# Performance work log

Hardware: AMD Instinct MI355X
Metric: run time of the kernel (lower is better)

The kernel has to match this reference:

```python
import jax, jax.numpy as jnp
import numpy as np

# ---- Haar DWT (levels=1, mode='zero'), matches pytorch_wavelets ordering ----
# For even H,W and filter length 2, zero-pad haar analysis reduces to
# non-overlapping 2x2 blocks. Subband order after the two 1D analyses
# (width first, then height): LL, (w-lo,h-hi), (w-hi,h-lo), HH.

def haar_dwt(x):
    a = x[..., 0::2, 0::2]
    b = x[..., 0::2, 1::2]
    c = x[..., 1::2, 0::2]
    d = x[..., 1::2, 1::2]
    ll = (a + b + c + d) * 0.5
    h0 = (a + b - c - d) * 0.5   # lo-width, hi-height
    h1 = (a - b + c - d) * 0.5   # hi-width, lo-height
    hh = (a - b - c + d) * 0.5
    return ll, jnp.stack([h0, h1, hh], axis=2)  # yh: (b,c,3,h/2,w/2)


def _interleave(u, v, axis):
    # interleave two equal-shaped arrays along `axis` (negative axis)
    s = list(u.shape)
    s[axis] *= 2
    return jnp.stack([u, v], axis=axis + len(u.shape) + 1).reshape(s)


def haar_idwt(ll, yh):
    h0, h1, hh = yh[:, :, 0], yh[:, :, 1], yh[:, :, 2]
    a = (ll + h0 + h1 + hh) * 0.5
    b = (ll + h0 - h1 - hh) * 0.5
    c = (ll - h0 + h1 - hh) * 0.5
    d = (ll - h0 - h1 + hh) * 0.5
    top = _interleave(a, b, -1)   # even rows
    bot = _interleave(c, d, -1)   # odd rows
    return _interleave(top, bot, -2)


def batched_dynamic_conv(feat, kernels, pad):
    """feat: (b,cin,h,w), kernels: (b,cout,cin,kh,kw) -> (b,cout,h,w).
    Per-sample kernels via grouped conv (batch as groups)."""
    bsz, cin, h, w = feat.shape
    cout, kh, kw = kernels.shape[1], kernels.shape[3], kernels.shape[4]
    lhs = feat.reshape(1, bsz * cin, h, w)
    rhs = kernels.reshape(bsz * cout, cin, kh, kw)
    out = jax.lax.conv_general_dilated(
        lhs, rhs, window_strides=(1, 1), padding=[(pad, pad), (pad, pad)],
        dimension_numbers=('NCHW', 'OIHW', 'NCHW'), feature_group_count=bsz)
    return out.reshape(bsz, cout, h, w)


def _dyn_conv_subband(feat, sub_kernels, attn_w, attn_b, pad=1):
    # attention: 1x1 conv -> global avg pool -> softmax over kernel_num
    logits = jnp.einsum('bchw,kc->bk', feat, attn_w) / (feat.shape[-2] * feat.shape[-1]) + attn_b
    att = jax.nn.softmax(logits, axis=1)                       # (b,K)
    kernels = jnp.einsum('bk,koiuv->boiuv', att, sub_kernels)  # (b,cout,cin,kh,kw)
    return batched_dynamic_conv(feat, kernels, pad)


def setup_inputs() -> dict:
    key = jax.random.key(0)
    k1, k2, k3, k4 = jax.random.split(key, 4)
    B, C, H, W = 8, 64, 128, 128
    K, SUB, COUT, KS = 4, 4, 64, 3  # kernel_num, 1+3*levels, out_channels, kernel_size
    return {
        'x': jax.random.normal(k1, (B, C, H, W), dtype=jnp.float32),
        'wt_kernels': jax.random.normal(k2, (K, SUB, COUT, C, KS, KS), dtype=jnp.float32) * 0.02,
        'attn_w': jax.random.normal(k3, (K, C), dtype=jnp.float32) * 0.1,
        'attn_b': jnp.zeros((K,), dtype=jnp.float32),
    }


def reference(x, wt_kernels, attn_w, attn_b):
    ll, yh = haar_dwt(x)
    subbands = [ll, yh[:, :, 0], yh[:, :, 1], yh[:, :, 2]]
    outs = [_dyn_conv_subband(sb, wt_kernels[:, i], attn_w, attn_b, pad=1)
            for i, sb in enumerate(subbands)]
    rec_yh = jnp.stack(outs[1:4], axis=2)  # (b,cout,3,h/2,w/2)
    return haar_idwt(outs[0], rec_yh)
```

## Files before the change

kernel.cpp:

```cpp
#include <hip/hip_runtime.h>
#include <hip/hip_bf16.h>
#include <math.h>


typedef __bf16 bf16x8 __attribute__((ext_vector_type(8)));
typedef float f32x4 __attribute__((ext_vector_type(4)));

__device__ __forceinline__ bf16x8 as_bf16x8(uint4 u) {
    union { uint4 a; bf16x8 b; } c; c.a = u; return c.b;
}
__device__ __forceinline__ unsigned short bf16bits(float f) {
    __hip_bfloat16 h = __float2bfloat16(f);
    union { __hip_bfloat16 h; unsigned short u; } c; c.h = h; return c.u;
}

__global__ __launch_bounds__(256)
void dwt_kernel(const float* __restrict__ x, const float* __restrict__ attn_w,
                unsigned short* __restrict__ feats, float* __restrict__ plog) {
    __shared__ uint4 sT[2304];
    __shared__ float sred[64][4];
    unsigned short* sTu = (unsigned short*)sT;
    int y = blockIdx.x, b = blockIdx.y;
    int t = threadIdx.x;
    int c = t >> 2, q = t & 3;

    const float4* r0 = (const float4*)x + ((size_t)(b * 64 + c) * 128 + 2 * y) * 32;
    const float4* r1 = r0 + 32;

    float s0 = 0.f, s1 = 0.f, s2 = 0.f, s3 = 0.f;
    #pragma unroll
    for (int i = 0; i < 8; ++i) {
        int f = i * 4 + q;
        float4 p = r0[f], qq = r1[f];
        int xo = 2 * f;
        {
            float a = p.x, bb = p.y, cc = qq.x, dd = qq.y;
            float ll = (a + bb + cc + dd) * 0.5f, h0 = (a + bb - cc - dd) * 0.5f;
            float h1 = (a - bb + cc - dd) * 0.5f, hh = (a - bb - cc + dd) * 0.5f;
            s0 += ll; s1 += h0; s2 += h1; s3 += hh;
            sTu[0 * 4608 + xo * 72 + c] = bf16bits(ll);
            sTu[1 * 4608 + xo * 72 + c] = bf16bits(h0);
            sTu[2 * 4608 + xo * 72 + c] = bf16bits(h1);
            sTu[3 * 4608 + xo * 72 + c] = bf16bits(hh);
        }
        {
            float a = p.z, bb = p.w, cc = qq.z, dd = qq.w;
            float ll = (a + bb + cc + dd) * 0.5f, h0 = (a + bb - cc - dd) * 0.5f;
            float h1 = (a - bb + cc - dd) * 0.5f, hh = (a - bb - cc + dd) * 0.5f;
            s0 += ll; s1 += h0; s2 += h1; s3 += hh;
            sTu[0 * 4608 + (xo + 1) * 72 + c] = bf16bits(ll);
            sTu[1 * 4608 + (xo + 1) * 72 + c] = bf16bits(h0);
            sTu[2 * 4608 + (xo + 1) * 72 + c] = bf16bits(h1);
            sTu[3 * 4608 + (xo + 1) * 72 + c] = bf16bits(hh);
        }
    }
    s0 += __shfl_xor(s0, 1); s0 += __shfl_xor(s0, 2);
    s1 += __shfl_xor(s1, 1); s1 += __shfl_xor(s1, 2);
    s2 += __shfl_xor(s2, 1); s2 += __shfl_xor(s2, 2);
    s3 += __shfl_xor(s3, 1); s3 += __shfl_xor(s3, 2);
    if (q == 0) { sred[c][0] = s0; sred[c][1] = s1; sred[c][2] = s2; sred[c][3] = s3; }
    __syncthreads();
    if (t < 16) {
        int sub = t >> 2, k = t & 3;
        float acc = 0.f;
        #pragma unroll 8
        for (int cc = 0; cc < 64; ++cc)
            acc += attn_w[k * 64 + cc] * sred[cc][sub];
        plog[((size_t)(b * 4 + sub) * 4 + k) * 64 + y] = acc;
    }
    uint4* fch = (uint4*)feats;
    for (int e = t; e < 2048; e += 256) {
        int s = e >> 9, xx = (e >> 3) & 63, ck = e & 7;
        fch[(size_t)((b * 4 + s) * 64 + y) * 512 + xx * 8 + ck] = sT[s * 576 + xx * 9 + ck];
    }
}

__global__ __launch_bounds__(256)
void mix_kernel(const float* __restrict__ wt, const float* __restrict__ attn_b,
                const float* __restrict__ plog, unsigned short* __restrict__ wmix) {
    __shared__ float sLw[4][576];
    __shared__ float satt[8][4];
    int co = blockIdx.x, sub = blockIdx.y;
    int t = threadIdx.x;

    if (t < 32) {
        int b = t >> 2, k = t & 3;
        const float* pp = plog + ((size_t)(b * 4 + sub) * 4 + k) * 64;
        float acc = 0.f;
        #pragma unroll 8
        for (int yy = 0; yy < 64; ++yy) acc += pp[yy];
        float logit = acc * (1.0f / 4096.0f) + attn_b[k];
        float m = fmaxf(logit, __shfl_xor(logit, 1));
        m = fmaxf(m, __shfl_xor(m, 2));
        float e = expf(logit - m);
        float s = e + __shfl_xor(e, 1);
        s += __shfl_xor(s, 2);
        satt[b][k] = e / s;
    }
    for (int e = t; e < 2304; e += 256) {
        int k = e / 576, r = e - k * 576;
        sLw[k][r] = wt[((size_t)(k * 4 + sub) * 64 + co) * 576 + r];
    }
    __syncthreads();
    #pragma unroll
    for (int j = 0; j < 18; ++j) {
        int idx = j * 256 + t;
        int b = idx / 576;
        int r = idx - b * 576;
        int tap = r >> 6, ci = r & 63;
        int wi = ci * 9 + tap;
        float v = satt[b][0] * sLw[0][wi] + satt[b][1] * sLw[1][wi]
                + satt[b][2] * sLw[2][wi] + satt[b][3] * sLw[3][wi];
        wmix[((size_t)(b * 4 + sub) * 9 + tap) * 4096 + co * 64 + ci] = bf16bits(v);
    }
}

__global__ __launch_bounds__(256, 2)
void conv_idwt_kernel(const unsigned short* __restrict__ feats,
                      const unsigned short* __restrict__ wmix,
                      float* __restrict__ out) {
    __shared__ uint4 sA[2592];
    __shared__ uint4 sW[1152];
    int cg = blockIdx.x, tile = blockIdx.y, b = blockIdx.z;
    int y0 = (tile >> 2) * 16, x0 = (tile & 3) * 16;
    int t = threadIdx.x, w = t >> 6, l = t & 63;
    int l16 = l & 15, kg = l >> 4;
    int w4 = w * 4;
    const uint4* fchb = (const uint4*)feats + (size_t)b * 131072;
    const uint4* wchb = (const uint4*)wmix + (size_t)b * 18432;

    f32x4 acc[4][4];
    #pragma unroll
    for (int s = 0; s < 4; ++s)
        #pragma unroll
        for (int r = 0; r < 4; ++r)
            acc[s][r] = (f32x4){0.f, 0.f, 0.f, 0.f};

    #pragma unroll
    for (int sp = 0; sp < 2; ++sp) {
        #pragma unroll
        for (int ck8 = 0; ck8 < 8; ck8 += 4) {
            __syncthreads();
            for (int e = t; e < 2592; e += 256) {
                int s2 = e / 1296, rr = e - s2 * 1296;
                int py = rr / 72, r2 = rr - py * 72, px = r2 >> 2, g = r2 & 3;
                int gy = y0 - 1 + py, gx = x0 - 1 + px;
                uint4 v = make_uint4(0u, 0u, 0u, 0u);
                if ((unsigned)gy < 64u && (unsigned)gx < 64u)
                    v = fchb[(size_t)(sp * 2 + s2) * 32768 + (gy * 64 + gx) * 8 + ck8 + g];
                sA[e] = v;
            }
            for (int e = t; e < 1152; e += 256) {
                int s2 = e / 576, r = e - s2 * 576;
                int tap = r >> 6, co = (r >> 2) & 15, g = r & 3;
                sW[e] = wchb[(size_t)(sp * 2 + s2) * 4608 + tap * 512
                             + (cg * 16 + co) * 8 + ck8 + g];
            }
            __syncthreads();
            #pragma unroll
            for (int s2 = 0; s2 < 2; ++s2) {
                int s = sp * 2 + s2;
                int abase = s2 * 1296;
                uint4 af[4][3];
                #pragma unroll
                for (int i = 0; i < 4; ++i)
                    #pragma unroll
                    for (int dx = 0; dx < 3; ++dx)
                        af[i][dx] = sA[abase + ((w4 + i) * 18 + l16 + dx) * 4 + kg];
                #pragma unroll
                for (int dy = 0; dy < 3; ++dy) {
                    if (dy > 0) {
                        #pragma unroll
                        for (int i = 0; i < 3; ++i)
                            #pragma unroll
                            for (int dx = 0; dx < 3; ++dx)
                                af[i][dx] = af[i + 1][dx];
                        #pragma unroll
                        for (int dx = 0; dx < 3; ++dx)
                            af[3][dx] = sA[abase + ((w4 + dy + 3) * 18 + l16 + dx) * 4 + kg];
                    }
                    #pragma unroll
                    for (int dx = 0; dx < 3; ++dx) {
                        uint4 bw = sW[s2 * 576 + (dy * 3 + dx) * 64 + l16 * 4 + kg];
                        bf16x8 bfr = as_bf16x8(bw);
                        #pragma unroll
                        for (int r = 0; r < 4; ++r)
                            acc[s][r] = __builtin_amdgcn_mfma_f32_16x16x32_bf16(
                                as_bf16x8(af[r][dx]), bfr, acc[s][r], 0, 0, 0);
                    }
                }
            }
        }
    }
    int co = cg * 16 + l16;
    #pragma unroll
    for (int r = 0; r < 4; ++r) {
        int ys = y0 + w4 + r;
        float* orow = out + ((size_t)(b * 64 + co) * 128 + 2 * ys) * 128 + 2 * x0 + 8 * kg;
        float av[4], bv[4], cv[4], dv[4];
        #pragma unroll
        for (int j = 0; j < 4; ++j) {
            float ll = acc[0][r][j], h0 = acc[1][r][j];
            float h1 = acc[2][r][j], hh = acc[3][r][j];
            av[j] = (ll + h0 + h1 + hh) * 0.5f;
            bv[j] = (ll + h0 - h1 - hh) * 0.5f;
            cv[j] = (ll - h0 + h1 - hh) * 0.5f;
            dv[j] = (ll - h0 - h1 + hh) * 0.5f;
        }
        *(float4*)(orow)           = make_float4(av[0], bv[0], av[1], bv[1]);
        *(float4*)(orow + 4)       = make_float4(av[2], bv[2], av[3], bv[3]);
        *(float4*)(orow + 128)     = make_float4(cv[0], dv[0], cv[1], dv[1]);
        *(float4*)(orow + 132)     = make_float4(cv[2], dv[2], cv[3], dv[3]);
    }
}

extern "C" void kernel_launch(void* const* d_in, const int* in_sizes, int n_in,
                              void* d_out, int out_size, void* d_ws, size_t ws_size,
                              hipStream_t stream) {
    const float* x  = (const float*)d_in[0];
    const float* wt = (const float*)d_in[1];
    const float* aw = (const float*)d_in[2];
    const float* ab = (const float*)d_in[3];
    float* out = (float*)d_out;
    char* ws = (char*)d_ws;

    float* plog              = (float*)ws;
    unsigned short* feats    = (unsigned short*)(ws + 32768);
    unsigned short* wmix     = (unsigned short*)(ws + 32768 + 16777216);

    hipLaunchKernelGGL(dwt_kernel, dim3(64, 8), dim3(256), 0, stream, x, aw, feats, plog);
    hipLaunchKernelGGL(mix_kernel, dim3(64, 4), dim3(256), 0, stream, wt, ab, plog, wmix);
    hipLaunchKernelGGL(conv_idwt_kernel, dim3(4, 16, 8), dim3(256), 0, stream,
                       feats, wmix, out);
}
```

Baseline: 133.5 us.

## Prefetch next conv stage into registers while computing current stage

Measured after the change: 134.7 us. Within noise of the previous version (+0.9%).

```diff
diff --git a/kernel.cpp b/kernel.cpp
--- a/kernel.cpp
+++ b/kernel.cpp
@@ -136,58 +136,102 @@
         for (int r = 0; r < 4; ++r)
             acc[s][r] = (f32x4){0.f, 0.f, 0.f, 0.f};
 
-    #pragma unroll
-    for (int sp = 0; sp < 2; ++sp) {
-        #pragma unroll
-        for (int ck8 = 0; ck8 < 8; ck8 += 4) {
-            __syncthreads();
-            for (int e = t; e < 2592; e += 256) {
-                int s2 = e / 1296, rr = e - s2 * 1296;
-                int py = rr / 72, r2 = rr - py * 72, px = r2 >> 2, g = r2 & 3;
-                int gy = y0 - 1 + py, gx = x0 - 1 + px;
+    int adec_py[11], adec_gx[11], adec_off[11];
+    int adec_s2[11];
+    bool a_ok[11];
+    #pragma unroll
+    for (int i = 0; i < 11; ++i) {
+        int e = t + i * 256;
+        if (e < 2592) {
+            int s2 = e / 1296, rr = e - s2 * 1296;
+            int py = rr / 72, r2 = rr - py * 72, px = r2 >> 2, g = r2 & 3;
+            int gy = y0 - 1 + py, gx = x0 - 1 + px;
+            adec_s2[i] = s2;
+            a_ok[i] = ((unsigned)gy < 64u) && ((unsigned)gx < 64u);
+            adec_off[i] = (gy * 64 + gx) * 8 + g;
+            adec_py[i] = 0; adec_gx[i] = 0;
+        } else { a_ok[i] = false; adec_s2[i] = 0; adec_off[i] = 0; }
+    }
+    int wdec_s2[5], wdec_off[5];
+    #pragma unroll
+    for (int i = 0; i < 5; ++i) {
+        int e = t + i * 256;
+        if (e < 1152) {
+            int s2 = e / 576, r = e - s2 * 576;
+            int tap = r >> 6, co = (r >> 2) & 15, g = r & 3;
+            wdec_s2[i] = s2;
+            wdec_off[i] = tap * 512 + (cg * 16 + co) * 8 + g;
+        } else { wdec_s2[i] = 0; wdec_off[i] = -1; }
+    }
+
+    uint4 ra[11], rw[5];
+    {
+        const int sp = 0, ck8 = 0;
+        #pragma unroll
+        for (int i = 0; i < 11; ++i) {
+            uint4 v = make_uint4(0u, 0u, 0u, 0u);
+            if (a_ok[i])
+                v = fchb[(size_t)(sp * 2 + adec_s2[i]) * 32768 + adec_off[i] + ck8];
+            ra[i] = v;
+        }
+        #pragma unroll
+        for (int i = 0; i < 5; ++i)
+            if (wdec_off[i] >= 0)
+                rw[i] = wchb[(size_t)(sp * 2 + wdec_s2[i]) * 4608 + wdec_off[i] + ck8];
+    }
+
+    #pragma unroll
+    for (int stg = 0; stg < 4; ++stg) {
+        __syncthreads();
+        #pragma unroll
+        for (int i = 0; i < 11; ++i) { int e = t + i * 256; if (e < 2592) sA[e] = ra[i]; }
+        #pragma unroll
+        for (int i = 0; i < 5; ++i)  { int e = t + i * 256; if (e < 1152) sW[e] = rw[i]; }
+        __syncthreads();
+        if (stg < 3) {
+            const int sp = (stg + 1) >> 1, ck8 = ((stg + 1) & 1) * 4;
+            #pragma unroll
+            for (int i = 0; i < 11; ++i) {
                 uint4 v = make_uint4(0u, 0u, 0u, 0u);
-                if ((unsigned)gy < 64u && (unsigned)gx < 64u)
-                    v = fchb[(size_t)(sp * 2 + s2) * 32768 + (gy * 64 + gx) * 8 + ck8 + g];
-                sA[e] = v;
+                if (a_ok[i])
+                    v = fchb[(size_t)(sp * 2 + adec_s2[i]) * 32768 + adec_off[i] + ck8];
+                ra[i] = v;
             }
-            for (int e = t; e < 1152; e += 256) {
-                int s2 = e / 576, r = e - s2 * 576;
-                int tap = r >> 6, co = (r >> 2) & 15, g = r & 3;
-                sW[e] = wchb[(size_t)(sp * 2 + s2) * 4608 + tap * 512
-                             + (cg * 16 + co) * 8 + ck8 + g];
-            }
-            __syncthreads();
-            #pragma unroll
-            for (int s2 = 0; s2 < 2; ++s2) {
-                int s = sp * 2 + s2;
-                int abase = s2 * 1296;
-                uint4 af[4][3];
+            #pragma unroll
+            for (int i = 0; i < 5; ++i)
+                if (wdec_off[i] >= 0)
+                    rw[i] = wchb[(size_t)(sp * 2 + wdec_s2[i]) * 4608 + wdec_off[i] + ck8];
+        }
+        #pragma unroll
+        for (int s2 = 0; s2 < 2; ++s2) {
+            const int sidx = (stg >> 1) * 2 + s2;
+            int abase = s2 * 1296;
+            uint4 af[4][3];
+            #pragma unroll
+            for (int i = 0; i < 4; ++i)
                 #pragma unroll
-                for (int i = 0; i < 4; ++i)
+                for (int dx = 0; dx < 3; ++dx)
+                    af[i][dx] = sA[abase + ((w4 + i) * 18 + l16 + dx) * 4 + kg];
+            #pragma unroll
+            for (int dy = 0; dy < 3; ++dy) {
+                if (dy > 0) {
+                    #pragma unroll
+                    for (int i = 0; i < 3; ++i)
+                        #pragma unroll
+                        for (int dx = 0; dx < 3; ++dx)
+                            af[i][dx] = af[i + 1][dx];
                     #pragma unroll
                     for (int dx = 0; dx < 3; ++dx)
-                        af[i][dx] = sA[abase + ((w4 + i) * 18 + l16 + dx) * 4 + kg];
+                        af[3][dx] = sA[abase + ((w4 + dy + 3) * 18 + l16 + dx) * 4 + kg];
+                }
                 #pragma unroll
-                for (int dy = 0; dy < 3; ++dy) {
-                    if (dy > 0) {
-                        #pragma unroll
-                        for (int i = 0; i < 3; ++i)
-                            #pragma unroll
-                            for (int dx = 0; dx < 3; ++dx)
-                                af[i][dx] = af[i + 1][dx];
-                        #pragma unroll
-                        for (int dx = 0; dx < 3; ++dx)
-                            af[3][dx] = sA[abase + ((w4 + dy + 3) * 18 + l16 + dx) * 4 + kg];
-                    }
+                for (int dx = 0; dx < 3; ++dx) {
+                    uint4 bw = sW[s2 * 576 + (dy * 3 + dx) * 64 + l16 * 4 + kg];
+                    bf16x8 bfr = as_bf16x8(bw);
                     #pragma unroll
-                    for (int dx = 0; dx < 3; ++dx) {
-                        uint4 bw = sW[s2 * 576 + (dy * 3 + dx) * 64 + l16 * 4 + kg];
-                        bf16x8 bfr = as_bf16x8(bw);
-                        #pragma unroll
-                        for (int r = 0; r < 4; ++r)
-                            acc[s][r] = __builtin_amdgcn_mfma_f32_16x16x32_bf16(
-                                as_bf16x8(af[r][dx]), bfr, acc[s][r], 0, 0, 0);
-                    }
+                    for (int r = 0; r < 4; ++r)
+                        acc[sidx][r] = __builtin_amdgcn_mfma_f32_16x16x32_bf16(
+                            as_bf16x8(af[r][dx]), bfr, acc[sidx][r], 0, 0, 0);
                 }
             }
         }
```

## Pre-pad DWT feature planes and stream conv tiles via direct global-to-LDS loads

Applied to the files above, without the earlier changes.

Measured after the change: 123.2 us. 1.08x faster.

```diff
diff --git a/kernel.cpp b/kernel.cpp
--- a/kernel.cpp
+++ b/kernel.cpp
@@ -13,6 +13,14 @@
     __hip_bfloat16 h = __float2bfloat16(f);
     union { __hip_bfloat16 h; unsigned short u; } c; c.h = h; return c.u;
 }
+__device__ __forceinline__ void gload_lds16(const uint4* g, uint4* l) {
+    __builtin_amdgcn_global_load_lds(
+        (const __attribute__((address_space(1))) unsigned int*)g,
+        (__attribute__((address_space(3))) unsigned int*)l, 16, 0, 0);
+}
+
+#define FPLANE 34848
+#define FROW   528
 
 __global__ __launch_bounds__(256)
 void dwt_kernel(const float* __restrict__ x, const float* __restrict__ attn_w,
@@ -68,10 +76,25 @@
             acc += attn_w[k * 64 + cc] * sred[cc][sub];
         plog[((size_t)(b * 4 + sub) * 4 + k) * 64 + y] = acc;
     }
-    uint4* fch = (uint4*)feats;
-    for (int e = t; e < 2048; e += 256) {
-        int s = e >> 9, xx = (e >> 3) & 63, ck = e & 7;
-        fch[(size_t)((b * 4 + s) * 64 + y) * 512 + xx * 8 + ck] = sT[s * 576 + xx * 9 + ck];
+    uint4* fpad = (uint4*)feats;
+    const uint4 zz = make_uint4(0u, 0u, 0u, 0u);
+    for (int e = t; e < 2112; e += 256) {
+        int s = e / 528, r = e - s * 528;
+        int px = r >> 3, ck = r & 7;
+        uint4 v = zz;
+        if (px >= 1 && px <= 64) v = sT[s * 576 + (px - 1) * 9 + ck];
+        fpad[((size_t)(b * 4 + s) * 66 + (y + 1)) * FROW + r] = v;
+    }
+    if (y == 0) {
+        for (int e = t; e < 2112; e += 256) {
+            int s = e / 528, r = e - s * 528;
+            fpad[(size_t)(b * 4 + s) * 66 * FROW + r] = zz;
+        }
+    } else if (y == 63) {
+        for (int e = t; e < 2112; e += 256) {
+            int s = e / 528, r = e - s * 528;
+            fpad[((size_t)(b * 4 + s) * 66 + 65) * FROW + r] = zz;
+        }
     }
 }
 
@@ -115,19 +138,21 @@
     }
 }
 
-__global__ __launch_bounds__(256, 2)
+__global__ __launch_bounds__(256, 3)
 void conv_idwt_kernel(const unsigned short* __restrict__ feats,
                       const unsigned short* __restrict__ wmix,
                       float* __restrict__ out) {
-    __shared__ uint4 sA[2592];
-    __shared__ uint4 sW[1152];
-    int cg = blockIdx.x, tile = blockIdx.y, b = blockIdx.z;
+    __shared__ uint4 sA[1296];
+    __shared__ uint4 sW[576];
+    int cg = blockIdx.x;
+    int tile = blockIdx.y;
+    int b = blockIdx.z;
     int y0 = (tile >> 2) * 16, x0 = (tile & 3) * 16;
     int t = threadIdx.x, w = t >> 6, l = t & 63;
     int l16 = l & 15, kg = l >> 4;
     int w4 = w * 4;
-    const uint4* fchb = (const uint4*)feats + (size_t)b * 131072;
-    const uint4* wchb = (const uint4*)wmix + (size_t)b * 18432;
+    const uint4* fpb  = (const uint4*)feats + (size_t)b * 4 * FPLANE;
+    const uint4* wchb = (const uint4*)wmix + (size_t)b * 4 * 4608;
 
     f32x4 acc[4][4];
     #pragma unroll
@@ -137,57 +162,60 @@
             acc[s][r] = (f32x4){0.f, 0.f, 0.f, 0.f};
 
     #pragma unroll
-    for (int sp = 0; sp < 2; ++sp) {
+    for (int sub = 0; sub < 4; ++sub) {
+        const uint4* fp  = fpb + (size_t)sub * FPLANE;
+        const uint4* wch = wchb + (size_t)sub * 4608;
         #pragma unroll
         for (int ck8 = 0; ck8 < 8; ck8 += 4) {
             __syncthreads();
-            for (int e = t; e < 2592; e += 256) {
-                int s2 = e / 1296, rr = e - s2 * 1296;
-                int py = rr / 72, r2 = rr - py * 72, px = r2 >> 2, g = r2 & 3;
-                int gy = y0 - 1 + py, gx = x0 - 1 + px;
-                uint4 v = make_uint4(0u, 0u, 0u, 0u);
-                if ((unsigned)gy < 64u && (unsigned)gx < 64u)
-                    v = fchb[(size_t)(sp * 2 + s2) * 32768 + (gy * 64 + gx) * 8 + ck8 + g];
-                sA[e] = v;
-            }
-            for (int e = t; e < 1152; e += 256) {
-                int s2 = e / 576, r = e - s2 * 576;
-                int tap = r >> 6, co = (r >> 2) & 15, g = r & 3;
-                sW[e] = wchb[(size_t)(sp * 2 + s2) * 4608 + tap * 512
-                             + (cg * 16 + co) * 8 + ck8 + g];
+            #pragma unroll
+            for (int i = 0; i < 5; ++i) {
+                int e = t + i * 256;
+                int py = e / 72, rr = e - py * 72, px = rr >> 2, g = rr & 3;
+                gload_lds16(fp + (size_t)((y0 + py) * 66 + x0 + px) * 8 + ck8 + g, &sA[e]);
+            }
+            if (t < 16) {
+                int e = 1280 + t;
+                int rr = e - 1224, px = rr >> 2, g = rr & 3;
+                sA[e] = fp[(size_t)((y0 + 17) * 66 + x0 + px) * 8 + ck8 + g];
+            }
+            #pragma unroll
+            for (int i = 0; i < 2; ++i) {
+                int e = t + i * 256;
+                int tap = e >> 6, rr = e & 63, co = rr >> 2, g = rr & 3;
+                gload_lds16(wch + tap * 512 + (cg * 16 + co) * 8 + ck8 + g, &sW[e]);
+            }
+            if (t < 64) {
+                int e = 512 + t;
+                int tap = e >> 6, rr = e & 63, co = rr >> 2, g = rr & 3;
+                gload_lds16(wch + tap * 512 + (cg * 16 + co) * 8 + ck8 + g, &sW[e]);
             }
             __syncthreads();
-            #pragma unroll
-            for (int s2 = 0; s2 < 2; ++s2) {
-                int s = sp * 2 + s2;
-                int abase = s2 * 1296;
-                uint4 af[4][3];
+            uint4 af[4][3];
+            #pragma unroll
+            for (int i = 0; i < 4; ++i)
                 #pragma unroll
-                for (int i = 0; i < 4; ++i)
+                for (int dx = 0; dx < 3; ++dx)
+                    af[i][dx] = sA[((w4 + i) * 18 + l16 + dx) * 4 + kg];
+            #pragma unroll
+            for (int dy = 0; dy < 3; ++dy) {
+                if (dy > 0) {
+                    #pragma unroll
+                    for (int i = 0; i < 3; ++i)
+                        #pragma unroll
+                        for (int dx = 0; dx < 3; ++dx)
+                            af[i][dx] = af[i + 1][dx];
                     #pragma unroll
                     for (int dx = 0; dx < 3; ++dx)
-                        af[i][dx] = sA[abase + ((w4 + i) * 18 + l16 + dx) * 4 + kg];
+                        af[3][dx] = sA[((w4 + dy + 3) * 18 + l16 + dx) * 4 + kg];
+                }
                 #pragma unroll
-                for (int dy = 0; dy < 3; ++dy) {
-                    if (dy > 0) {
-                        #pragma unroll
-                        for (int i = 0; i < 3; ++i)
-                            #pragma unroll
-                            for (int dx = 0; dx < 3; ++dx)
-                                af[i][dx] = af[i + 1][dx];
-                        #pragma unroll
-                        for (int dx = 0; dx < 3; ++dx)
-                            af[3][dx] = sA[abase + ((w4 + dy + 3) * 18 + l16 + dx) * 4 + kg];
-                    }
+                for (int dx = 0; dx < 3; ++dx) {
+                    bf16x8 bw = as_bf16x8(sW[(dy * 3 + dx) * 64 + l16 * 4 + kg]);
                     #pragma unroll
-                    for (int dx = 0; dx < 3; ++dx) {
-                        uint4 bw = sW[s2 * 576 + (dy * 3 + dx) * 64 + l16 * 4 + kg];
-                        bf16x8 bfr = as_bf16x8(bw);
-                        #pragma unroll
-                        for (int r = 0; r < 4; ++r)
-                            acc[s][r] = __builtin_amdgcn_mfma_f32_16x16x32_bf16(
-                                as_bf16x8(af[r][dx]), bfr, acc[s][r], 0, 0, 0);
-                    }
+                    for (int r = 0; r < 4; ++r)
+                        acc[sub][r] = __builtin_amdgcn_mfma_f32_16x16x32_bf16(
+                            as_bf16x8(af[r][dx]), bw, acc[sub][r], 0, 0, 0);
                 }
             }
         }
@@ -207,10 +235,10 @@
             cv[j] = (ll - h0 + h1 - hh) * 0.5f;
             dv[j] = (ll - h0 - h1 + hh) * 0.5f;
         }
-        *(float4*)(orow)           = make_float4(av[0], bv[0], av[1], bv[1]);
-        *(float4*)(orow + 4)       = make_float4(av[2], bv[2], av[3], bv[3]);
-        *(float4*)(orow + 128)     = make_float4(cv[0], dv[0], cv[1], dv[1]);
-        *(float4*)(orow + 132)     = make_float4(cv[2], dv[2], cv[3], dv[3]);
+        *(float4*)(orow)       = make_float4(av[0], bv[0], av[1], bv[1]);
+        *(float4*)(orow + 4)   = make_float4(av[2], bv[2], av[3], bv[3]);
+        *(float4*)(orow + 128) = make_float4(cv[0], dv[0], cv[1], dv[1]);
+        *(float4*)(orow + 132) = make_float4(cv[2], dv[2], cv[3], dv[3]);
     }
 }
 
@@ -224,9 +252,9 @@
     float* out = (float*)d_out;
     char* ws = (char*)d_ws;
 
-    float* plog              = (float*)ws;
-    unsigned short* feats    = (unsigned short*)(ws + 32768);
-    unsigned short* wmix     = (unsigned short*)(ws + 32768 + 16777216);
+    float* plog           = (float*)ws;
+    unsigned short* feats = (unsigned short*)(ws + 32768);
+    unsigned short* wmix  = (unsigned short*)(ws + 32768 + 17842176);
 
     hipLaunchKernelGGL(dwt_kernel, dim3(64, 8), dim3(256), 0, stream, x, aw, feats, plog);
     hipLaunchKernelGGL(mix_kernel, dim3(64, 4), dim3(256), 0, stream, wt, ab, plog, wmix);
```
